# Kernel tuning notes

Hardware: AMD Instinct MI355X
Metric: run time of the kernel (lower is better)

## Reference

```python
import jax, jax.numpy as jnp
import numpy as np

B, S, D = 8, 4096, 512
L = 8921  # n_labels (ICD9 full)

def setup_inputs() -> dict:
    key = jax.random.key(0)
    kx, ku = jax.random.split(key)
    x = jax.random.normal(kx, (B, S, D), dtype=jnp.float32)
    # xavier_uniform init for U [L, D]
    bound = jnp.sqrt(6.0 / (L + D)).astype(jnp.float32)
    U = jax.random.uniform(ku, (L, D), dtype=jnp.float32, minval=-bound, maxval=bound)
    return {"x": x, "U": U}

def reference(x, U):
    # scores: [B, L, S] = U @ x^T (unscaled)
    scores = jnp.einsum('ld,bsd->bls', U, x)
    alpha = jax.nn.softmax(scores, axis=2)  # softmax over sequence dim
    out = jnp.einsum('bls,bsd->bld', alpha, x)  # [B, L, D]
    return (out, alpha)
```

## Files before the change

### kernel.cpp

```cpp
#include <hip/hip_runtime.h>
#include <stdint.h>
#include <stddef.h>

#define BB 8
#define SS 4096
#define DD 512
#define LL 8921

typedef __attribute__((ext_vector_type(8))) short bf16x8;
typedef __attribute__((ext_vector_type(4))) float f32x4;
typedef __attribute__((ext_vector_type(4))) unsigned short u16x4;
typedef __attribute__((ext_vector_type(8))) unsigned short u16x8;

__device__ __forceinline__ unsigned short f2bf(float f) {
  union { float f; uint32_t u; } v; v.f = f;
  uint32_t r = (v.u + 0x7FFFu + ((v.u >> 16) & 1u)) >> 16;
  return (unsigned short)r;
}

__device__ __forceinline__ float bf2f(unsigned short h) {
  union { uint32_t u; float f; } v; v.u = ((uint32_t)h) << 16;
  return v.f;
}

__device__ __forceinline__ void gload_lds16(const void* g, void* l) {
  __builtin_amdgcn_global_load_lds(
      (__attribute__((address_space(1))) void*)(void*)g,
      (__attribute__((address_space(3))) void*)l, 16, 0, 0);
}

__device__ __forceinline__ f32x4 mfma16(bf16x8 a, bf16x8 b, f32x4 c) {
  return __builtin_amdgcn_mfma_f32_16x16x32_bf16(a, b, c, 0, 0, 0);
}

__global__ __launch_bounds__(256) void k_cvtU(const float* __restrict__ U,
                                              unsigned short* __restrict__ Ub) {
  const int idx = blockIdx.x * 256 + threadIdx.x;
  const int nchunk = (LL * DD) / 8;
  if (idx >= nchunk) return;
  const float4* s = (const float4*)U + (size_t)idx * 2;
  const float4 a = s[0], b = s[1];
  u16x8 h;
  h[0] = f2bf(a.x); h[1] = f2bf(a.y); h[2] = f2bf(a.z); h[3] = f2bf(a.w);
  h[4] = f2bf(b.x); h[5] = f2bf(b.y); h[6] = f2bf(b.z); h[7] = f2bf(b.w);
  *(u16x8*)(Ub + (size_t)idx * 8) = h;
}

__global__ __launch_bounds__(256) void k_cvtx(const float* __restrict__ x,
                                              unsigned short* __restrict__ xb,
                                              unsigned short* __restrict__ xT) {
  __shared__ unsigned short t[64][72];
  const int b = blockIdx.z;
  const int s0 = blockIdx.x * 64;
  const int d0 = blockIdx.y * 64;
  const int tid = threadIdx.x;
  const int rr = tid >> 4;
  const int cv = tid & 15;
#pragma unroll
  for (int i = 0; i < 4; ++i) {
    const int srow = rr + i * 16;
    const size_t gi = ((size_t)b * SS + s0 + srow) * DD + d0 + cv * 4;
    const float4 v = *(const float4*)&x[gi];
    u16x4 h;
    h[0] = f2bf(v.x); h[1] = f2bf(v.y); h[2] = f2bf(v.z); h[3] = f2bf(v.w);
    *(u16x4*)&xb[gi] = h;
    t[srow][cv * 4 + 0] = h[0]; t[srow][cv * 4 + 1] = h[1];
    t[srow][cv * 4 + 2] = h[2]; t[srow][cv * 4 + 3] = h[3];
  }
  __syncthreads();
#pragma unroll
  for (int i = 0; i < 4; ++i) {
    const int drow = rr + i * 16;
    u16x4 h;
    h[0] = t[cv * 4 + 0][drow]; h[1] = t[cv * 4 + 1][drow];
    h[2] = t[cv * 4 + 2][drow]; h[3] = t[cv * 4 + 3][drow];
    *(u16x4*)&xT[((size_t)b * DD + d0 + drow) * SS + s0 + cv * 4] = h;
  }
}


__global__ __launch_bounds__(256) void k_score2(const unsigned short* __restrict__ Ub,
                                                const unsigned short* __restrict__ xb,
                                                unsigned short* __restrict__ es,
                                                float* __restrict__ Z) {
  __shared__ unsigned short smem[2][128][64];
  const int tid = threadIdx.x;
  const int lane = tid & 63, wid = tid >> 6;
  const int wr = wid >> 1, wc = wid & 1;
  const int b = blockIdx.y;
  const int lt = blockIdx.x >> 5, st = blockIdx.x & 31;
  const int l0 = lt * 128, s0 = st * 128;
  const int fr = lane & 15, fq = lane >> 4;

  f32x4 acc[4][4];
#pragma unroll
  for (int m = 0; m < 4; ++m)
#pragma unroll
    for (int n = 0; n < 4; ++n) acc[m][n] = (f32x4){0.f, 0.f, 0.f, 0.f};

  for (int k0 = 0; k0 < DD; k0 += 64) {
#pragma unroll
    for (int r = 0; r < 4; ++r) {
      const int c = r * 256 + tid;
      const int row = c >> 3, col = (c & 7) * 8;
      int lrow = l0 + row; if (lrow > LL - 1) lrow = LL - 1;
      gload_lds16(Ub + (size_t)lrow * DD + k0 + col, (unsigned short*)smem[0] + c * 8);
      gload_lds16(xb + ((size_t)b * SS + s0 + row) * DD + k0 + col,
                  (unsigned short*)smem[1] + c * 8);
    }
    __syncthreads();
#pragma unroll
    for (int kk = 0; kk < 64; kk += 32) {
      bf16x8 af[4], bfv[4];
#pragma unroll
      for (int m = 0; m < 4; ++m)
        af[m] = *(const bf16x8*)&smem[0][wr * 64 + m * 16 + fr][kk + fq * 8];
#pragma unroll
      for (int n = 0; n < 4; ++n)
        bfv[n] = *(const bf16x8*)&smem[1][wc * 64 + n * 16 + fr][kk + fq * 8];
#pragma unroll
      for (int m = 0; m < 4; ++m)
#pragma unroll
        for (int n = 0; n < 4; ++n)
          acc[m][n] = mfma16(af[m], bfv[n], acc[m][n]);
    }
    __syncthreads();
  }

  float ev[4][4][4];
  float rsum[4][4];
#pragma unroll
  for (int m = 0; m < 4; ++m)
#pragma unroll
    for (int j = 0; j < 4; ++j) rsum[m][j] = 0.f;
#pragma unroll
  for (int m = 0; m < 4; ++m)
#pragma unroll
    for (int n = 0; n < 4; ++n)
#pragma unroll
      for (int j = 0; j < 4; ++j) {
        const float e = __expf(acc[m][n][j]);
        ev[m][n][j] = e;
        rsum[m][j] += e;
      }
#pragma unroll
  for (int m = 0; m < 4; ++m)
#pragma unroll
    for (int j = 0; j < 4; ++j) {
      float v = rsum[m][j];
      v += __shfl_xor(v, 1);
      v += __shfl_xor(v, 2);
      v += __shfl_xor(v, 4);
      v += __shfl_xor(v, 8);
      const int l = l0 + wr * 64 + m * 16 + fq * 4 + j;
      if (fr == 0 && l < LL) atomicAdd(&Z[b * LL + l], v);
    }
  unsigned short (*Es)[128] = (unsigned short (*)[128])smem;
#pragma unroll
  for (int m = 0; m < 4; ++m) {
    const int lr = wr * 64 + m * 16 + fq * 4;
#pragma unroll
    for (int n = 0; n < 4; ++n) {
      const int sc = wc * 64 + n * 16 + fr;
#pragma unroll
      for (int j = 0; j < 4; ++j) {
        const int ll = lr + j;
        Es[ll][sc ^ ((ll & 7) << 3)] = f2bf(ev[m][n][j]);
      }
    }
  }
  __syncthreads();
  {
    const int lr = tid >> 1;
    const int ch = (tid & 1) * 64;
    const int l = l0 + lr;
    if (l < LL) {
      unsigned short* dst = es + ((size_t)b * LL + l) * SS + s0 + ch;
#pragma unroll
      for (int w = 0; w < 8; ++w) {
        u16x8 hv = *(const u16x8*)&Es[lr][(ch + w * 8) ^ ((lr & 7) << 3)];
        *(u16x8*)(dst + w * 8) = hv;
      }
    }
  }
}

__global__ __launch_bounds__(256) void k_pv3(const unsigned short* __restrict__ es,
                                             const unsigned short* __restrict__ xTb,
                                             const float* __restrict__ Z,
                                             float* __restrict__ out,
                                             float* __restrict__ alpha) {
  __shared__ unsigned short As[128][64];
  __shared__ unsigned short Bs[128][64];
  const int tid = threadIdx.x;
  const int lane = tid & 63, wid = tid >> 6;
  const int wr = wid >> 1, wc = wid & 1;
  const int b = blockIdx.y;
  const int bid = blockIdx.x;
  const int logical = (bid & 7) * 35 + (bid >> 3);
  const int lt = logical >> 2, dt = logical & 3;
  const int l0 = lt * 128, d0 = dt * 128;
  const int fr = lane & 15, fq = lane >> 4;

  float rZrow[4];
#pragma unroll
  for (int r = 0; r < 4; ++r) {
    int lrow = l0 + r * 32 + (tid >> 3);
    if (lrow > LL - 1) lrow = LL - 1;
    rZrow[r] = 1.0f / Z[b * LL + lrow];
  }

  f32x4 acc[4][4];
#pragma unroll
  for (int m = 0; m < 4; ++m)
#pragma unroll
    for (int n = 0; n < 4; ++n) acc[m][n] = (f32x4){0.f, 0.f, 0.f, 0.f};

  for (int k0 = 0; k0 < SS; k0 += 64) {
#pragma unroll
    for (int r = 0; r < 4; ++r) {
      const int c = r * 256 + tid;
      const int row = c >> 3, col = (c & 7) * 8;
      int lrow = l0 + row; if (lrow > LL - 1) lrow = LL - 1;
      gload_lds16(es + ((size_t)b * LL + lrow) * SS + k0 + col,
                  (unsigned short*)As + c * 8);
      gload_lds16(xTb + ((size_t)b * DD + d0 + row) * SS + k0 + col,
                  (unsigned short*)Bs + c * 8);
    }
    __syncthreads();

    if (dt == 0) {
#pragma unroll
      for (int r = 0; r < 4; ++r) {
        const int c = r * 256 + tid;
        const int row = c >> 3, col = (c & 7) * 8;
        int lrow = l0 + row; if (lrow > LL - 1) lrow = LL - 1;
        const u16x8 h = *(const u16x8*)((unsigned short*)As + c * 8);
        const float rz = rZrow[r];
        float4 a, bv;
        a.x = bf2f(h[0]) * rz; a.y = bf2f(h[1]) * rz;
        a.z = bf2f(h[2]) * rz; a.w = bf2f(h[3]) * rz;
        bv.x = bf2f(h[4]) * rz; bv.y = bf2f(h[5]) * rz;
        bv.z = bf2f(h[6]) * rz; bv.w = bf2f(h[7]) * rz;
        float* dst = alpha + ((size_t)b * LL + lrow) * SS + k0 + col;
        *(float4*)dst = a;
        *(float4*)(dst + 4) = bv;
      }
    }

#pragma unroll
    for (int kk = 0; kk < 64; kk += 32) {
      bf16x8 af[4], bfv[4];
#pragma unroll
      for (int m = 0; m < 4; ++m)
        af[m] = *(const bf16x8*)&As[wr * 64 + m * 16 + fr][kk + fq * 8];
#pragma unroll
      for (int n = 0; n < 4; ++n)
        bfv[n] = *(const bf16x8*)&Bs[wc * 64 + n * 16 + fr][kk + fq * 8];
#pragma unroll
      for (int m = 0; m < 4; ++m)
#pragma unroll
        for (int n = 0; n < 4; ++n)
          acc[m][n] = mfma16(af[m], bfv[n], acc[m][n]);
    }
    __syncthreads();
  }

  float rZv[4][4];
#pragma unroll
  for (int m = 0; m < 4; ++m)
#pragma unroll
    for (int j = 0; j < 4; ++j) {
      const int l = l0 + wr * 64 + m * 16 + fq * 4 + j;
      rZv[m][j] = (l < LL) ? (1.0f / Z[b * LL + l]) : 0.f;
    }
#pragma unroll
  for (int m = 0; m < 4; ++m) {
    const int lbase = l0 + wr * 64 + m * 16 + fq * 4;
#pragma unroll
    for (int n = 0; n < 4; ++n) {
      const int d = d0 + wc * 64 + n * 16 + fr;
#pragma unroll
      for (int j = 0; j < 4; ++j) {
        const int l = lbase + j;
        if (l < LL) out[((size_t)b * LL + l) * DD + d] = acc[m][n][j] * rZv[m][j];
      }
    }
  }
}


__global__ __launch_bounds__(256) void k_score(const unsigned short* __restrict__ Ub,
                                               const unsigned short* __restrict__ xb,
                                               float* __restrict__ alpha,
                                               float* __restrict__ Z) {
  __shared__ unsigned short As[128][64];
  __shared__ unsigned short Bs[128][64];
  const int tid = threadIdx.x;
  const int lane = tid & 63, wid = tid >> 6;
  const int wr = wid >> 1, wc = wid & 1;
  const int b = blockIdx.y;
  const int lt = blockIdx.x >> 5, st = blockIdx.x & 31;
  const int l0 = lt * 128, s0 = st * 128;
  const int fr = lane & 15, fq = lane >> 4;

  f32x4 acc[4][4];
#pragma unroll
  for (int m = 0; m < 4; ++m)
#pragma unroll
    for (int n = 0; n < 4; ++n) acc[m][n] = (f32x4){0.f, 0.f, 0.f, 0.f};

  for (int k0 = 0; k0 < DD; k0 += 64) {
#pragma unroll
    for (int r = 0; r < 4; ++r) {
      const int c = r * 256 + tid;
      const int row = c >> 3, col = (c & 7) * 8;
      int lrow = l0 + row; if (lrow > LL - 1) lrow = LL - 1;
      gload_lds16(Ub + (size_t)lrow * DD + k0 + col, (unsigned short*)As + c * 8);
      gload_lds16(xb + ((size_t)b * SS + s0 + row) * DD + k0 + col,
                  (unsigned short*)Bs + c * 8);
    }
    __syncthreads();
#pragma unroll
    for (int kk = 0; kk < 64; kk += 32) {
      bf16x8 af[4], bfv[4];
#pragma unroll
      for (int m = 0; m < 4; ++m)
        af[m] = *(const bf16x8*)&As[wr * 64 + m * 16 + fr][kk + fq * 8];
#pragma unroll
      for (int n = 0; n < 4; ++n)
        bfv[n] = *(const bf16x8*)&Bs[wc * 64 + n * 16 + fr][kk + fq * 8];
#pragma unroll
      for (int m = 0; m < 4; ++m)
#pragma unroll
        for (int n = 0; n < 4; ++n)
          acc[m][n] = mfma16(af[m], bfv[n], acc[m][n]);
    }
    __syncthreads();
  }

  float rsum[4][4];
#pragma unroll
  for (int m = 0; m < 4; ++m)
#pragma unroll
    for (int j = 0; j < 4; ++j) rsum[m][j] = 0.f;
#pragma unroll
  for (int m = 0; m < 4; ++m) {
    const int lbase = l0 + wr * 64 + m * 16 + fq * 4;
#pragma unroll
    for (int n = 0; n < 4; ++n) {
      const int s = s0 + wc * 64 + n * 16 + fr;
#pragma unroll
      for (int j = 0; j < 4; ++j) {
        const float e = __expf(acc[m][n][j]);
        rsum[m][j] += e;
        const int l = lbase + j;
        if (l < LL) alpha[((size_t)b * LL + l) * SS + s] = e;
      }
    }
  }
#pragma unroll
  for (int m = 0; m < 4; ++m)
#pragma unroll
    for (int j = 0; j < 4; ++j) {
      float v = rsum[m][j];
      v += __shfl_xor(v, 1);
      v += __shfl_xor(v, 2);
      v += __shfl_xor(v, 4);
      v += __shfl_xor(v, 8);
      const int l = l0 + wr * 64 + m * 16 + fq * 4 + j;
      if (fr == 0 && l < LL) atomicAdd(&Z[b * LL + l], v);
    }
}

__global__ __launch_bounds__(256) void k_scale(float* __restrict__ alpha,
                                               const float* __restrict__ Z) {
  const int row = blockIdx.x;
  const float rZ = 1.0f / Z[row];
  float4* p = (float4*)alpha + (size_t)row * (SS / 4);
  const int t = threadIdx.x;
#pragma unroll
  for (int i = 0; i < 4; ++i) {
    float4 v = p[t + i * 256];
    v.x *= rZ; v.y *= rZ; v.z *= rZ; v.w *= rZ;
    p[t + i * 256] = v;
  }
}

__global__ __launch_bounds__(256) void k_pv(const float* __restrict__ alpha,
                                            const unsigned short* __restrict__ xTb,
                                            float* __restrict__ out) {
  __shared__ unsigned short As[128][64];
  __shared__ unsigned short Bs[128][64];
  const int tid = threadIdx.x;
  const int lane = tid & 63, wid = tid >> 6;
  const int wr = wid >> 1, wc = wid & 1;
  const int b = blockIdx.y;
  const int lt = blockIdx.x >> 2, dt = blockIdx.x & 3;
  const int l0 = lt * 128, d0 = dt * 128;
  const int fr = lane & 15, fq = lane >> 4;

  f32x4 acc[4][4];
#pragma unroll
  for (int m = 0; m < 4; ++m)
#pragma unroll
    for (int n = 0; n < 4; ++n) acc[m][n] = (f32x4){0.f, 0.f, 0.f, 0.f};

  for (int k0 = 0; k0 < SS; k0 += 64) {
#pragma unroll
    for (int r = 0; r < 4; ++r) {
      const int c = r * 256 + tid;
      const int row = c >> 3, col = (c & 7) * 8;
      gload_lds16(xTb + ((size_t)b * DD + d0 + row) * SS + k0 + col,
                  (unsigned short*)Bs + c * 8);
      int lrow = l0 + row; if (lrow > LL - 1) lrow = LL - 1;
      const float* src = alpha + ((size_t)b * LL + lrow) * SS + k0 + col;
      const float4 v0 = *(const float4*)src;
      const float4 v1 = *(const float4*)(src + 4);
      bf16x8 h;
      h[0] = (short)f2bf(v0.x); h[1] = (short)f2bf(v0.y);
      h[2] = (short)f2bf(v0.z); h[3] = (short)f2bf(v0.w);
      h[4] = (short)f2bf(v1.x); h[5] = (short)f2bf(v1.y);
      h[6] = (short)f2bf(v1.z); h[7] = (short)f2bf(v1.w);
      *(bf16x8*)((unsigned short*)As + c * 8) = h;
    }
    __syncthreads();
#pragma unroll
    for (int kk = 0; kk < 64; kk += 32) {
      bf16x8 af[4], bfv[4];
#pragma unroll
      for (int m = 0; m < 4; ++m)
        af[m] = *(const bf16x8*)&As[wr * 64 + m * 16 + fr][kk + fq * 8];
#pragma unroll
      for (int n = 0; n < 4; ++n)
        bfv[n] = *(const bf16x8*)&Bs[wc * 64 + n * 16 + fr][kk + fq * 8];
#pragma unroll
      for (int m = 0; m < 4; ++m)
#pragma unroll
        for (int n = 0; n < 4; ++n)
          acc[m][n] = mfma16(af[m], bfv[n], acc[m][n]);
    }
    __syncthreads();
  }

#pragma unroll
  for (int m = 0; m < 4; ++m) {
    const int lbase = l0 + wr * 64 + m * 16 + fq * 4;
#pragma unroll
    for (int n = 0; n < 4; ++n) {
      const int d = d0 + wc * 64 + n * 16 + fr;
#pragma unroll
      for (int j = 0; j < 4; ++j) {
        const int l = lbase + j;
        if (l < LL) out[((size_t)b * LL + l) * DD + d] = acc[m][n][j];
      }
    }
  }
}

extern "C" void kernel_launch(void* const* d_in, const int* in_sizes, int n_in,
                              void* d_out, int out_size, void* d_ws, size_t ws_size,
                              hipStream_t stream) {
  const float* x = (const float*)d_in[0];
  const float* U = (const float*)d_in[1];
  float* out   = (float*)d_out;
  float* alpha = out + (size_t)BB * LL * DD;

  const size_t off_Z  = 0;
  const size_t off_U  = 285696;
  const size_t off_xb = 9420800;
  const size_t off_xT = 42975232;
  const size_t off_es = 76529664;
  const size_t es_bytes = (size_t)BB * LL * SS * 2;
  const size_t need_small = off_es;
  const size_t need_big   = off_es + es_bytes;

  if (ws_size < need_small) return;

  char* ws = (char*)d_ws;
  float* Z = (float*)(ws + off_Z);
  unsigned short* Ub = (unsigned short*)(ws + off_U);
  unsigned short* xb = (unsigned short*)(ws + off_xb);
  unsigned short* xT = (unsigned short*)(ws + off_xT);
  unsigned short* es = (unsigned short*)(ws + off_es);

  hipMemsetAsync(Z, 0, (size_t)BB * LL * 4, stream);
  k_cvtU<<<dim3(((LL * DD / 8) + 255) / 256), 256, 0, stream>>>(U, Ub);
  k_cvtx<<<dim3(SS / 64, DD / 64, BB), 256, 0, stream>>>(x, xb, xT);

  if (ws_size >= need_big) {
    k_score2<<<dim3(70 * 32, BB), 256, 0, stream>>>(Ub, xb, es, Z);
    k_pv3<<<dim3(70 * 4, BB), 256, 0, stream>>>(es, xT, Z, out, alpha);
  } else {
    k_score<<<dim3(70 * 32, BB), 256, 0, stream>>>(Ub, xb, alpha, Z);
    k_scale<<<dim3(BB * LL), 256, 0, stream>>>(alpha, Z);
    k_pv<<<dim3(70 * 4, BB), 256, 0, stream>>>(alpha, xT, out);
  }
}
```

Baseline: 1.544 ms.

## Double-buffer PV kernel LDS tiles and spread alpha writes across d-tiles

The PV GEMM kernel now uses two LDS buffers, prefetching the next K tile via direct global-to-LDS loads while MFMAs run on the current one. It syncs once per step with an explicit vmcnt wait and barrier, and raises wave priority around the MFMA section. The normalized alpha output writes, previously done only by d-tile 0 blocks, are now split so each of the four d-tile blocks writes a quarter of the K range. This aims to hide load latency and balance the heavy fp32 alpha store traffic, at the cost of doubled LDS usage, which may reduce occupancy.

Result: faster. 1.490 ms (-3.5%).

```diff
diff --git a/kernel.cpp b/kernel.cpp
--- a/kernel.cpp
+++ b/kernel.cpp
@@ -185,13 +185,13 @@
   }
 }
 
-__global__ __launch_bounds__(256) void k_pv3(const unsigned short* __restrict__ es,
+__global__ __launch_bounds__(256) void k_pv5(const unsigned short* __restrict__ es,
                                              const unsigned short* __restrict__ xTb,
                                              const float* __restrict__ Z,
                                              float* __restrict__ out,
                                              float* __restrict__ alpha) {
-  __shared__ unsigned short As[128][64];
-  __shared__ unsigned short Bs[128][64];
+  __shared__ unsigned short As[2][128][64];
+  __shared__ unsigned short Bs[2][128][64];
   const int tid = threadIdx.x;
   const int lane = tid & 63, wid = tid >> 6;
   const int wr = wid >> 1, wc = wid & 1;
@@ -205,7 +205,7 @@
   float rZrow[4];
 #pragma unroll
   for (int r = 0; r < 4; ++r) {
-    int lrow = l0 + r * 32 + (tid >> 3);
+    int lrow = l0 + ((r * 256 + tid) >> 3);
     if (lrow > LL - 1) lrow = LL - 1;
     rZrow[r] = 1.0f / Z[b * LL + lrow];
   }
@@ -216,26 +216,31 @@
 #pragma unroll
     for (int n = 0; n < 4; ++n) acc[m][n] = (f32x4){0.f, 0.f, 0.f, 0.f};
 
-  for (int k0 = 0; k0 < SS; k0 += 64) {
+  auto STAGE = [&](unsigned short (*An)[64], unsigned short (*Bn)[64], int k0) {
 #pragma unroll
     for (int r = 0; r < 4; ++r) {
       const int c = r * 256 + tid;
       const int row = c >> 3, col = (c & 7) * 8;
       int lrow = l0 + row; if (lrow > LL - 1) lrow = LL - 1;
       gload_lds16(es + ((size_t)b * LL + lrow) * SS + k0 + col,
-                  (unsigned short*)As + c * 8);
+                  (unsigned short*)An + c * 8);
       gload_lds16(xTb + ((size_t)b * DD + d0 + row) * SS + k0 + col,
-                  (unsigned short*)Bs + c * 8);
-    }
-    __syncthreads();
-
-    if (dt == 0) {
+                  (unsigned short*)Bn + c * 8);
+    }
+  };
+
+  auto BODY = [&](int t, unsigned short (*Ac)[64], unsigned short (*Bc)[64],
+                  unsigned short (*An)[64], unsigned short (*Bn)[64]) {
+    if (t < 63) STAGE(An, Bn, (t + 1) * 64);
+
+    if ((t >> 4) == dt) {
+      const int k0 = t * 64;
 #pragma unroll
       for (int r = 0; r < 4; ++r) {
         const int c = r * 256 + tid;
         const int row = c >> 3, col = (c & 7) * 8;
         int lrow = l0 + row; if (lrow > LL - 1) lrow = LL - 1;
-        const u16x8 h = *(const u16x8*)((unsigned short*)As + c * 8);
+        const u16x8 h = *(const u16x8*)((unsigned short*)Ac + c * 8);
         const float rz = rZrow[r];
         float4 a, bv;
         a.x = bf2f(h[0]) * rz; a.y = bf2f(h[1]) * rz;
@@ -248,22 +253,39 @@
       }
     }
 
+    __builtin_amdgcn_s_setprio(1);
 #pragma unroll
     for (int kk = 0; kk < 64; kk += 32) {
       bf16x8 af[4], bfv[4];
 #pragma unroll
       for (int m = 0; m < 4; ++m)
-        af[m] = *(const bf16x8*)&As[wr * 64 + m * 16 + fr][kk + fq * 8];
+        af[m] = *(const bf16x8*)&Ac[wr * 64 + m * 16 + fr][kk + fq * 8];
 #pragma unroll
       for (int n = 0; n < 4; ++n)
-        bfv[n] = *(const bf16x8*)&Bs[wc * 64 + n * 16 + fr][kk + fq * 8];
+        bfv[n] = *(const bf16x8*)&Bc[wc * 64 + n * 16 + fr][kk + fq * 8];
 #pragma unroll
       for (int m = 0; m < 4; ++m)
 #pragma unroll
         for (int n = 0; n < 4; ++n)
           acc[m][n] = mfma16(af[m], bfv[n], acc[m][n]);
     }
-    __syncthreads();
+    __builtin_amdgcn_s_setprio(0);
+
+    if (t < 63) {
+      __builtin_amdgcn_sched_barrier(0);
+      asm volatile("s_waitcnt vmcnt(0)" ::: "memory");
+      __builtin_amdgcn_s_barrier();
+      __builtin_amdgcn_sched_barrier(0);
+    }
+  };
+
+  STAGE(As[0], Bs[0], 0);
+  asm volatile("s_waitcnt vmcnt(0)" ::: "memory");
+  __syncthreads();
+
+  for (int tt = 0; tt < 32; ++tt) {
+    BODY(2 * tt,     As[0], Bs[0], As[1], Bs[1]);
+    BODY(2 * tt + 1, As[1], Bs[1], As[0], Bs[0]);
   }
 
   float rZv[4][4];
@@ -490,7 +512,7 @@
 
   if (ws_size >= need_big) {
     k_score2<<<dim3(70 * 32, BB), 256, 0, stream>>>(Ub, xb, es, Z);
-    k_pv3<<<dim3(70 * 4, BB), 256, 0, stream>>>(es, xT, Z, out, alpha);
+    k_pv5<<<dim3(70 * 4, BB), 256, 0, stream>>>(es, xT, Z, out, alpha);
   } else {
     k_score<<<dim3(70 * 32, BB), 256, 0, stream>>>(Ub, xb, alpha, Z);
     k_scale<<<dim3(BB * LL), 256, 0, stream>>>(alpha, Z);
```
